# Kernel tuning notes

Measured on AMD Instinct MI355X. Metric: run time of the kernel, lower is better.

## Reference

```python
import jax, jax.numpy as jnp
import numpy as np

E, B, L, D = 3, 4, 1024, 768
DS = 64            # d_state
DI = 2 * D         # d_inner (expand=2)
DTR = 48           # dt_rank = ceil(D/16)
K = 4              # depthwise conv kernel size


def setup_inputs() -> dict:
    key = jax.random.key(0)
    ks = jax.random.split(key, 10)
    s = lambda i, shape, scale=0.02: (jax.random.normal(ks[i], shape, jnp.float32) * scale)
    A_log = jnp.broadcast_to(jnp.log(jnp.arange(1, DS + 1, dtype=jnp.float32)), (E, DI, DS))
    return {
        "base":   jax.random.normal(ks[0], (B, L, D), jnp.float32),
        "per_ch": jax.random.normal(ks[1], (E, B, L, D), jnp.float32),
        "alpha":  jnp.ones((E,), jnp.float32) / E,
        "ln_g":   jnp.ones((D,), jnp.float32),
        "ln_b":   jnp.zeros((D,), jnp.float32),
        "W_in":   s(2, (E, D, 2 * DI)),
        "conv_w": s(3, (E, DI, K), 0.1),
        "conv_b": jnp.zeros((E, DI), jnp.float32),
        "W_x":    s(4, (E, DI, DTR + 2 * DS)),
        "W_dt":   s(5, (E, DTR, DI), 0.05),
        "b_dt":   jnp.full((E, DI), -4.6, jnp.float32),  # softplus^-1(~0.01)
        "A_log":  A_log,
        "D_skip": jnp.ones((E, DI), jnp.float32),
        "W_out":  s(6, (E, DI, D)),
    }


def layer_norm(x, g, b, eps=1e-5):
    mu = jnp.mean(x, axis=-1, keepdims=True)
    var = jnp.mean(jnp.square(x - mu), axis=-1, keepdims=True)
    return (x - mu) * jax.lax.rsqrt(var + eps) * g + b


def mamba(x, W_in, conv_w, conv_b, W_x, W_dt, b_dt, A_log, D_skip, W_out):
    # x: [B, L, D]
    xz = x @ W_in                                   # [B, L, 2*DI]
    xp, z = jnp.split(xz, 2, axis=-1)               # each [B, L, DI]
    # causal depthwise conv along L
    xc = jnp.pad(xp, ((0, 0), (K - 1, 0), (0, 0)))
    xc = jax.lax.conv_general_dilated(
        jnp.swapaxes(xc, 1, 2),                     # [B, DI, L+K-1]
        conv_w[:, None, :],                         # [DI, 1, K]
        window_strides=(1,), padding='VALID',
        dimension_numbers=('NCH', 'OIH', 'NCH'),
        feature_group_count=DI)
    xc = jnp.swapaxes(xc, 1, 2) + conv_b            # [B, L, DI]
    xs = jax.nn.silu(xc)
    dbl = xs @ W_x                                  # [B, L, DTR+2*DS]
    dt, Bm, Cm = jnp.split(dbl, [DTR, DTR + DS], axis=-1)
    dt = jax.nn.softplus(dt @ W_dt + b_dt)          # [B, L, DI]
    A = -jnp.exp(A_log)                             # [DI, DS]

    def step(h, t):
        u_t, dt_t, B_t, C_t = t                     # [B,DI],[B,DI],[B,DS],[B,DS]
        dA = jnp.exp(dt_t[..., None] * A)           # [B, DI, DS]
        h = dA * h + (dt_t * u_t)[..., None] * B_t[:, None, :]
        y = jnp.einsum('bds,bs->bd', h, C_t)
        return h, y

    tm = lambda a: jnp.swapaxes(a, 0, 1)            # time-major
    h0 = jnp.zeros((x.shape[0], DI, DS), x.dtype)
    _, ys = jax.lax.scan(step, h0, (tm(xs), tm(dt), tm(Bm), tm(Cm)))
    y = jnp.swapaxes(ys, 0, 1) + xs * D_skip        # [B, L, DI]
    y = y * jax.nn.silu(z)
    return y @ W_out                                # [B, L, D]


def reference(base, per_ch, alpha, ln_g, ln_b, W_in, conv_w, conv_b, W_x,
              W_dt, b_dt, A_log, D_skip, W_out):
    w = jax.nn.softmax(alpha)                       # [E]
    xn = layer_norm(per_ch, ln_g, ln_b)             # shared LN on each channel
    outs = jax.vmap(mamba)(xn, W_in, conv_w, conv_b, W_x,
                           W_dt, b_dt, A_log, D_skip, W_out)  # [E, B, L, D]
    injection = jnp.einsum('e,ebld->bld', w, outs)
    return base + injection
```

## Files before the change

### kernel.cpp

```cpp
#include <hip/hip_runtime.h>
#include <hip/hip_bf16.h>

typedef __hip_bfloat16 bf16;
typedef unsigned short u16;
typedef __attribute__((ext_vector_type(8))) short s16x8;
typedef __attribute__((ext_vector_type(4))) short s16x4;
typedef __attribute__((ext_vector_type(4))) float f32x4;

#define EXP 3
#define BB  4
#define LL  1024
#define DD  768
#define DSN 64
#define DIN 1536
#define DTR 48
#define MM  4096

struct alignas(8)  bf16x4 { bf16 v[4]; };
struct alignas(16) bf16x8 { bf16 v[8]; };

__device__ __forceinline__ float siluf(float x) { return x / (1.f + __expf(-x)); }
__device__ __forceinline__ float softplusf(float x) { return (x > 15.f) ? x : log1pf(__expf(x)); }
__device__ __forceinline__ float bf2f(u16 h) { union { unsigned u; float f; } x; x.u = ((unsigned)h) << 16; return x.f; }

template <int CTRL>
__device__ __forceinline__ float ror_add(float x) {
  int y = __builtin_amdgcn_update_dpp(0, __float_as_int(x), CTRL, 0xf, 0xf, true);
  return x + __int_as_float(y);
}

__launch_bounds__(256)
__global__ void ln_apply_k(const float* __restrict__ pc, const float* __restrict__ lng,
                           const float* __restrict__ lnb, bf16* __restrict__ out) {
  int row  = blockIdx.x * 4 + (threadIdx.x >> 6);
  int lane = threadIdx.x & 63;
  const float* x = pc + (size_t)row * DD;
  float4 v[3];
  float s = 0.f, sq = 0.f;
#pragma unroll
  for (int i = 0; i < 3; i++) {
    v[i] = *(const float4*)(x + lane * 4 + i * 256);
    s  += v[i].x + v[i].y + v[i].z + v[i].w;
    sq += v[i].x * v[i].x + v[i].y * v[i].y + v[i].z * v[i].z + v[i].w * v[i].w;
  }
#pragma unroll
  for (int o = 1; o < 64; o <<= 1) { s += __shfl_xor(s, o); sq += __shfl_xor(sq, o); }
  float mu = s * (1.f / 768.f);
  float rs = rsqrtf(sq * (1.f / 768.f) - mu * mu + 1e-5f);
  bf16* op = out + (size_t)row * DD;
#pragma unroll
  for (int i = 0; i < 3; i++) {
    int col = lane * 4 + i * 256;
    float4 g4 = *(const float4*)(lng + col);
    float4 b4 = *(const float4*)(lnb + col);
    bf16x4 pk;
    pk.v[0] = (bf16)((v[i].x - mu) * rs * g4.x + b4.x);
    pk.v[1] = (bf16)((v[i].y - mu) * rs * g4.y + b4.y);
    pk.v[2] = (bf16)((v[i].z - mu) * rs * g4.z + b4.z);
    pk.v[3] = (bf16)((v[i].w - mu) * rs * g4.w + b4.w);
    *(bf16x4*)(op + col) = pk;
  }
}

__launch_bounds__(256)
__global__ void tcvt_k(const float* __restrict__ in, bf16* __restrict__ out,
                       int Ksrc, int ldin, int ldout,
                       size_t sIn, size_t sOut, int mode, const float* __restrict__ alphap) {
  __shared__ float tl[32][33];
  int z = blockIdx.z;
  const float* src = in + (size_t)z * sIn;
  bf16* dst = out + (size_t)z * sOut;
  int n0 = blockIdx.x * 32, k0 = blockIdx.y * 32;
  int tx = threadIdx.x, ty = threadIdx.y;
  int n = n0 + tx;
  int c = n; bool nv = true;
  if (mode == 1) {
    if (n < 48)       c = n;
    else if (n < 64)  nv = false;
    else if (n < 192) c = n - 16;
    else              nv = false;
  }
  float scale = 1.f;
  if (mode == 2) {
    float a0 = alphap[0], a1 = alphap[1], a2 = alphap[2];
    float mx = fmaxf(a0, fmaxf(a1, a2));
    float e0 = __expf(a0 - mx), e1 = __expf(a1 - mx), e2 = __expf(a2 - mx);
    scale = ((z == 0) ? e0 : (z == 1) ? e1 : e2) / (e0 + e1 + e2);
  }
#pragma unroll
  for (int i = 0; i < 32; i += 8) {
    int k = k0 + ty + i;
    float v = (nv && k < Ksrc) ? src[(size_t)k * ldin + c] : 0.f;
    tl[ty + i][tx] = v * scale;
  }
  __syncthreads();
#pragma unroll
  for (int i = 0; i < 32; i += 8) {
    dst[(size_t)(n0 + ty + i) * ldout + (k0 + tx)] = (bf16)tl[tx][ty + i];
  }
}

__launch_bounds__(256)
__global__ void conv_silu_k(const bf16* __restrict__ xp, const float* __restrict__ cw,
                            const float* __restrict__ cb, bf16* __restrict__ xs) {
  long i = ((long)blockIdx.x * 256 + threadIdx.x) * 8;
  int  c  = (int)(i % DIN);
  long rl = i / DIN;
  int  l  = (int)(rl & (LL - 1));
  int  e  = (int)(rl >> 12);
  const float* wp  = cw + (size_t)e * DIN * 4 + (size_t)c * 4;
  const float* cbp = cb + (size_t)e * DIN + c;
  float acc[8];
#pragma unroll
  for (int j = 0; j < 8; j++) acc[j] = cbp[j];
#pragma unroll
  for (int tap = 0; tap < 4; tap++) {
    if (l - 3 + tap >= 0) {
      s16x8 xv = *(const s16x8*)(const void*)(xp + (rl + tap - 3) * DIN + c);
#pragma unroll
      for (int j = 0; j < 8; j++)
        acc[j] = fmaf(bf2f((u16)xv[j]), wp[j * 4 + tap], acc[j]);
    }
  }
  bf16x8 pk;
#pragma unroll
  for (int j = 0; j < 8; j++) pk.v[j] = (bf16)siluf(acc[j]);
  *(bf16x8*)(xs + rl * DIN + c) = pk;
}

template<int MODE>
__launch_bounds__(256)
__global__ void mfma_gemm_k(const bf16* __restrict__ A, const bf16* __restrict__ Bt,
                            int Kdim, int lda,
                            size_t sA, size_t sB, size_t sO,
                            bf16* __restrict__ o0, bf16* __restrict__ o1,
                            const float* __restrict__ bias,
                            float* __restrict__ outp) {
  __shared__ short As[128 * 32];
  __shared__ short Bs[128 * 32];
  int z = blockIdx.z;
  A  += (size_t)z * sA;
  Bt += (size_t)z * sB;
  if (o0) o0 += (size_t)z * sO;
  if (o1) o1 += (size_t)z * sO;
  if constexpr (MODE == 1) outp += (size_t)z * (size_t)MM * 128;
  const float* bz = (MODE == 2) ? bias + (size_t)z * DIN : bias;

  int t = threadIdx.x;
  int l = t & 63, w = t >> 6;
  int wr = w >> 1, wc = w & 1;
  int n0 = blockIdx.x * 128, r0 = blockIdx.y * 128;

  int row = t >> 2, c3 = t & 3, col = c3 * 8;
  int plo = ((c3 & 1) ? 16 : 0) + ((c3 & 2) ? 4 : 0);
  int lrow = (l & 15) * 32 + (l >> 4) * 8;

  f32x4 acc[4][4] = {};

  for (int k0 = 0; k0 < Kdim; k0 += 32) {
    s16x8 va0 = *(const s16x8*)(const void*)(A  + (size_t)(r0 + row)      * lda  + k0 + col);
    s16x8 va1 = *(const s16x8*)(const void*)(A  + (size_t)(r0 + row + 64) * lda  + k0 + col);
    s16x8 vb0 = *(const s16x8*)(const void*)(Bt + (size_t)(n0 + row)      * Kdim + k0 + col);
    s16x8 vb1 = *(const s16x8*)(const void*)(Bt + (size_t)(n0 + row + 64) * Kdim + k0 + col);
    __syncthreads();
    *(s16x4*)(As + row * 32 + plo)          = __builtin_shufflevector(va0, va0, 0, 1, 2, 3);
    *(s16x4*)(As + row * 32 + plo + 8)      = __builtin_shufflevector(va0, va0, 4, 5, 6, 7);
    *(s16x4*)(As + (row + 64) * 32 + plo)     = __builtin_shufflevector(va1, va1, 0, 1, 2, 3);
    *(s16x4*)(As + (row + 64) * 32 + plo + 8) = __builtin_shufflevector(va1, va1, 4, 5, 6, 7);
    *(s16x4*)(Bs + row * 32 + plo)          = __builtin_shufflevector(vb0, vb0, 0, 1, 2, 3);
    *(s16x4*)(Bs + row * 32 + plo + 8)      = __builtin_shufflevector(vb0, vb0, 4, 5, 6, 7);
    *(s16x4*)(Bs + (row + 64) * 32 + plo)     = __builtin_shufflevector(vb1, vb1, 0, 1, 2, 3);
    *(s16x4*)(Bs + (row + 64) * 32 + plo + 8) = __builtin_shufflevector(vb1, vb1, 4, 5, 6, 7);
    __syncthreads();
    s16x8 af[4], bfv[4];
#pragma unroll
    for (int m = 0; m < 4; m++) af[m]  = *(const s16x8*)(As + (wr * 64 + m * 16) * 32 + lrow);
#pragma unroll
    for (int n = 0; n < 4; n++) bfv[n] = *(const s16x8*)(Bs + (wc * 64 + n * 16) * 32 + lrow);
#pragma unroll
    for (int m = 0; m < 4; m++)
#pragma unroll
      for (int n = 0; n < 4; n++)
        acc[m][n] = __builtin_amdgcn_mfma_f32_16x16x32_bf16(af[m], bfv[n], acc[m][n], 0, 0, 0);
  }

  int rb = r0 + wr * 64 + ((l >> 4) << 2);
  int cb = n0 + wc * 64 + (l & 15);
#pragma unroll
  for (int m = 0; m < 4; m++)
#pragma unroll
    for (int n = 0; n < 4; n++)
#pragma unroll
      for (int r = 0; r < 4; r++) {
        int gr = rb + m * 16 + r;
        int gc = cb + n * 16;
        float v = acc[m][n][r];
        if constexpr (MODE == 0) {
          if (n0 < DIN) o0[(size_t)gr * DIN + gc] = (bf16)v;
          else          o1[(size_t)gr * DIN + (gc - DIN)] = (bf16)siluf(v);
        } else if constexpr (MODE == 1) {
          if (gc < 64)       o0[(size_t)gr * 64 + gc] = (bf16)v;
          else if (gc < 192) outp[(size_t)gr * 128 + (gc - 64)] = v;
        } else if constexpr (MODE == 2) {
          o0[(size_t)gr * DIN + gc] = (bf16)softplusf(v + bz[gc]);
        } else {
          atomicAdd(&outp[(size_t)gr * DD + gc], v);
        }
      }
}

__launch_bounds__(256)
__global__ void copy4_k(const float* __restrict__ s, float* __restrict__ d, int n4) {
  int i = blockIdx.x * 256 + threadIdx.x;
  if (i < n4) ((float4*)d)[i] = ((const float4*)s)[i];
}

__launch_bounds__(256)
__global__ void scan_k(const bf16* __restrict__ dtb, bf16* __restrict__ xsb,
                       const bf16* __restrict__ gb, const float* __restrict__ dbl,
                       const float* __restrict__ A_log, const float* __restrict__ Dsk) {
  int gt = blockIdx.x * 256 + threadIdx.x;
  int sg = gt & 15;
  int cidx = gt >> 4;
  int d  = cidx % DIN;
  int eb = cidx / DIN;
  int e  = eb >> 2;

  float4 Ar = *(const float4*)(A_log + ((size_t)e * DIN + d) * DSN + sg * 4);
  const float LOG2E = 1.44269504088896f;
  float4 A2;
  A2.x = -__expf(Ar.x) * LOG2E;
  A2.y = -__expf(Ar.y) * LOG2E;
  A2.z = -__expf(Ar.z) * LOG2E;
  A2.w = -__expf(Ar.w) * LOG2E;
  float4 h = {0.f, 0.f, 0.f, 0.f};
  float dskip = Dsk[(size_t)e * DIN + d];

  unsigned idx  = (unsigned)eb * (LL * DIN) + (unsigned)d;
  unsigned bofs = (unsigned)eb * (LL * 128) + (unsigned)(sg * 4);

  float dtv = (float)dtb[idx];
  float u   = (float)xsb[idx];
  float gv  = (float)gb[idx];
  float4 Bv = *(const float4*)(dbl + bofs);
  float4 Cv = *(const float4*)(dbl + bofs + 64);

#pragma unroll 4
  for (int l = 0; l < LL; ++l) {
    unsigned idxn = idx + DIN;
    unsigned bofn = bofs + 128;
    float dtn = (float)dtb[idxn];
    float un  = (float)xsb[idxn];
    float gn  = (float)gb[idxn];
    float4 Bn = *(const float4*)(dbl + bofn);
    float4 Cn = *(const float4*)(dbl + bofn + 64);

    float du = dtv * u;
    float4 dA;
    dA.x = __builtin_amdgcn_exp2f(dtv * A2.x);
    dA.y = __builtin_amdgcn_exp2f(dtv * A2.y);
    dA.z = __builtin_amdgcn_exp2f(dtv * A2.z);
    dA.w = __builtin_amdgcn_exp2f(dtv * A2.w);
    h.x = fmaf(dA.x, h.x, du * Bv.x);
    h.y = fmaf(dA.y, h.y, du * Bv.y);
    h.z = fmaf(dA.z, h.z, du * Bv.z);
    h.w = fmaf(dA.w, h.w, du * Bv.w);
    float p = fmaf(h.x, Cv.x, fmaf(h.y, Cv.y, fmaf(h.z, Cv.z, h.w * Cv.w)));
    p = ror_add<0x128>(p);
    p = ror_add<0x124>(p);
    p = ror_add<0x122>(p);
    p = ror_add<0x121>(p);
    if (sg == 0) {
      xsb[idx] = (bf16)(fmaf(u, dskip, p) * gv);
    }
    idx = idxn; bofs = bofn;
    dtv = dtn; u = un; gv = gn; Bv = Bn; Cv = Cn;
  }
}

extern "C" void kernel_launch(void* const* d_in, const int* in_sizes, int n_in,
                              void* d_out, int out_size, void* d_ws, size_t ws_size,
                              hipStream_t stream) {
  const float* base   = (const float*)d_in[0];
  const float* per_ch = (const float*)d_in[1];
  const float* alpha  = (const float*)d_in[2];
  const float* ln_g   = (const float*)d_in[3];
  const float* ln_b   = (const float*)d_in[4];
  const float* W_in   = (const float*)d_in[5];
  const float* conv_w = (const float*)d_in[6];
  const float* conv_b = (const float*)d_in[7];
  const float* W_x    = (const float*)d_in[8];
  const float* W_dt   = (const float*)d_in[9];
  const float* b_dt   = (const float*)d_in[10];
  const float* A_log  = (const float*)d_in[11];
  const float* D_skip = (const float*)d_in[12];
  const float* W_out  = (const float*)d_in[13];
  float* out = (float*)d_out;
  (void)in_sizes; (void)n_in; (void)out_size; (void)ws_size;

  char* ws = (char*)d_ws;
  const size_t R = (size_t)EXP * MM * DIN * 2;
  bf16* Abf   = (bf16*)ws;
  bf16* xsws  = (bf16*)ws;
  bf16* gws   = (bf16*)(ws + R);
  bf16* dtws  = (bf16*)(ws + 2 * R);
  char* R4    = ws + 3 * R;
  bf16*  WinT  = (bf16*)R4;
  bf16*  WoutT = (bf16*)R4;
  float* dblf  = (float*)(R4 + 7077888);
  bf16* WxT   = (bf16*)(ws + 3 * R + 14155776);
  bf16* WdtT  = (bf16*)(ws + 3 * R + 14155776 + 2359296);
  bf16* dblp  = (bf16*)(ws + 3 * R + 14155776 + 2359296 + 589824);

  dim3 blk2(32, 8);

  ln_apply_k<<<EXP * BB * LL / 4, 256, 0, stream>>>(per_ch, ln_g, ln_b, Abf);
  tcvt_k<<<dim3(96, 24, EXP), blk2, 0, stream>>>(W_in, WinT, 768, 3072, 768,
        (size_t)768 * 3072, (size_t)3072 * 768, 0, nullptr);
  tcvt_k<<<dim3(8, 48, EXP), blk2, 0, stream>>>(W_x, WxT, 1536, 176, 1536,
        (size_t)1536 * 176, (size_t)256 * 1536, 1, nullptr);
  tcvt_k<<<dim3(48, 2, EXP), blk2, 0, stream>>>(W_dt, WdtT, 48, 1536, 64,
        (size_t)48 * 1536, (size_t)1536 * 64, 0, nullptr);

  mfma_gemm_k<0><<<dim3(24, 32, EXP), 256, 0, stream>>>(Abf, WinT, 768, DD,
        (size_t)MM * DD, (size_t)3072 * 768, (size_t)MM * DIN,
        dtws, gws, nullptr, nullptr);

  tcvt_k<<<dim3(24, 48, EXP), blk2, 0, stream>>>(W_out, WoutT, 1536, 768, 1536,
        (size_t)1536 * 768, (size_t)768 * 1536, 2, alpha);

  conv_silu_k<<<EXP * BB * LL * DIN / 8 / 256, 256, 0, stream>>>(dtws, conv_w, conv_b, xsws);

  mfma_gemm_k<1><<<dim3(2, 32, EXP), 256, 0, stream>>>(xsws, WxT, 1536, DIN,
        (size_t)MM * DIN, (size_t)256 * 1536, (size_t)MM * 64,
        dblp, nullptr, nullptr, dblf);

  mfma_gemm_k<2><<<dim3(12, 32, EXP), 256, 0, stream>>>(dblp, WdtT, 64, 64,
        (size_t)MM * 64, (size_t)1536 * 64, (size_t)MM * DIN,
        dtws, nullptr, b_dt, nullptr);

  copy4_k<<<MM * DD / 4 / 256, 256, 0, stream>>>(base, out, MM * DD / 4);
  scan_k<<<EXP * BB * DIN * 16 / 256, 256, 0, stream>>>(dtws, xsws, gws, dblf, A_log, D_skip);
  mfma_gemm_k<3><<<dim3(6, 32, EXP), 256, 0, stream>>>(xsws, WoutT, 1536, DIN,
        (size_t)MM * DIN, (size_t)768 * 1536, 0,
        nullptr, nullptr, nullptr, out);
}
```

Before: 898.3 us.

## Fuse silu(z) gating into output GEMM and deepen GEMM K-step to 64

The out-projection GEMM now multiplies its A tiles by the silu(z) gate while loading, so the scan kernel no longer reads the gate tensor each timestep. All MFMA GEMMs also stage 64-wide K slices per iteration instead of 32, halving the barrier and loop overhead per K. This doubles shared memory per block, raises register pressure and may lower occupancy. It also adds an extra bf16 rounding of the gated product.

```diff
diff --git a/kernel.cpp b/kernel.cpp
--- a/kernel.cpp
+++ b/kernel.cpp
@@ -22,6 +22,17 @@
 __device__ __forceinline__ float siluf(float x) { return x / (1.f + __expf(-x)); }
 __device__ __forceinline__ float softplusf(float x) { return (x > 15.f) ? x : log1pf(__expf(x)); }
 __device__ __forceinline__ float bf2f(u16 h) { union { unsigned u; float f; } x; x.u = ((unsigned)h) << 16; return x.f; }
+
+__device__ __forceinline__ s16x8 gmul8(s16x8 a, s16x8 g) {
+  s16x8 r;
+#pragma unroll
+  for (int j = 0; j < 8; j++) {
+    union { bf16 b; u16 u; } cv;
+    cv.b = (bf16)(bf2f((u16)a[j]) * bf2f((u16)g[j]));
+    r[j] = (short)cv.u;
+  }
+  return r;
+}
 
 template <int CTRL>
 __device__ __forceinline__ float ror_add(float x) {
@@ -135,15 +146,17 @@
                             size_t sA, size_t sB, size_t sO,
                             bf16* __restrict__ o0, bf16* __restrict__ o1,
                             const float* __restrict__ bias,
-                            float* __restrict__ outp) {
-  __shared__ short As[128 * 32];
-  __shared__ short Bs[128 * 32];
+                            float* __restrict__ outp,
+                            const bf16* __restrict__ gat) {
+  __shared__ short As[128 * 64];
+  __shared__ short Bs[128 * 64];
   int z = blockIdx.z;
   A  += (size_t)z * sA;
   Bt += (size_t)z * sB;
   if (o0) o0 += (size_t)z * sO;
   if (o1) o1 += (size_t)z * sO;
   if constexpr (MODE == 1) outp += (size_t)z * (size_t)MM * 128;
+  if constexpr (MODE == 3) gat += (size_t)z * sA;
   const float* bz = (MODE == 2) ? bias + (size_t)z * DIN : bias;
 
   int t = threadIdx.x;
@@ -157,32 +170,51 @@
 
   f32x4 acc[4][4] = {};
 
-  for (int k0 = 0; k0 < Kdim; k0 += 32) {
-    s16x8 va0 = *(const s16x8*)(const void*)(A  + (size_t)(r0 + row)      * lda  + k0 + col);
-    s16x8 va1 = *(const s16x8*)(const void*)(A  + (size_t)(r0 + row + 64) * lda  + k0 + col);
-    s16x8 vb0 = *(const s16x8*)(const void*)(Bt + (size_t)(n0 + row)      * Kdim + k0 + col);
-    s16x8 vb1 = *(const s16x8*)(const void*)(Bt + (size_t)(n0 + row + 64) * Kdim + k0 + col);
+#define PUT(DST, ROW, V)                                                        \
+  { *(s16x4*)((DST) + (ROW) * 32 + plo)     = __builtin_shufflevector(V, V, 0, 1, 2, 3); \
+    *(s16x4*)((DST) + (ROW) * 32 + plo + 8) = __builtin_shufflevector(V, V, 4, 5, 6, 7); }
+
+  for (int k0 = 0; k0 < Kdim; k0 += 64) {
+    const bf16* pa = A  + (size_t)(r0 + row) * lda  + k0 + col;
+    const bf16* pb = Bt + (size_t)(n0 + row) * Kdim + k0 + col;
+    s16x8 va0 = *(const s16x8*)(const void*)(pa);
+    s16x8 va1 = *(const s16x8*)(const void*)(pa + (size_t)64 * lda);
+    s16x8 va2 = *(const s16x8*)(const void*)(pa + 32);
+    s16x8 va3 = *(const s16x8*)(const void*)(pa + (size_t)64 * lda + 32);
+    s16x8 vb0 = *(const s16x8*)(const void*)(pb);
+    s16x8 vb1 = *(const s16x8*)(const void*)(pb + (size_t)64 * Kdim);
+    s16x8 vb2 = *(const s16x8*)(const void*)(pb + 32);
+    s16x8 vb3 = *(const s16x8*)(const void*)(pb + (size_t)64 * Kdim + 32);
+    if constexpr (MODE == 3) {
+      const bf16* pg = gat + (size_t)(r0 + row) * lda + k0 + col;
+      va0 = gmul8(va0, *(const s16x8*)(const void*)(pg));
+      va1 = gmul8(va1, *(const s16x8*)(const void*)(pg + (size_t)64 * lda));
+      va2 = gmul8(va2, *(const s16x8*)(const void*)(pg + 32));
+      va3 = gmul8(va3, *(const s16x8*)(const void*)(pg + (size_t)64 * lda + 32));
+    }
     __syncthreads();
-    *(s16x4*)(As + row * 32 + plo)          = __builtin_shufflevector(va0, va0, 0, 1, 2, 3);
-    *(s16x4*)(As + row * 32 + plo + 8)      = __builtin_shufflevector(va0, va0, 4, 5, 6, 7);
-    *(s16x4*)(As + (row + 64) * 32 + plo)     = __builtin_shufflevector(va1, va1, 0, 1, 2, 3);
-    *(s16x4*)(As + (row + 64) * 32 + plo + 8) = __builtin_shufflevector(va1, va1, 4, 5, 6, 7);
-    *(s16x4*)(Bs + row * 32 + plo)          = __builtin_shufflevector(vb0, vb0, 0, 1, 2, 3);
-    *(s16x4*)(Bs + row * 32 + plo + 8)      = __builtin_shufflevector(vb0, vb0, 4, 5, 6, 7);
-    *(s16x4*)(Bs + (row + 64) * 32 + plo)     = __builtin_shufflevector(vb1, vb1, 0, 1, 2, 3);
-    *(s16x4*)(Bs + (row + 64) * 32 + plo + 8) = __builtin_shufflevector(vb1, vb1, 4, 5, 6, 7);
+    PUT(As, row, va0)  PUT(As, row + 64, va1)
+    PUT(As + 4096, row, va2)  PUT(As + 4096, row + 64, va3)
+    PUT(Bs, row, vb0)  PUT(Bs, row + 64, vb1)
+    PUT(Bs + 4096, row, vb2)  PUT(Bs + 4096, row + 64, vb3)
     __syncthreads();
-    s16x8 af[4], bfv[4];
-#pragma unroll
-    for (int m = 0; m < 4; m++) af[m]  = *(const s16x8*)(As + (wr * 64 + m * 16) * 32 + lrow);
-#pragma unroll
-    for (int n = 0; n < 4; n++) bfv[n] = *(const s16x8*)(Bs + (wc * 64 + n * 16) * 32 + lrow);
-#pragma unroll
-    for (int m = 0; m < 4; m++)
-#pragma unroll
-      for (int n = 0; n < 4; n++)
-        acc[m][n] = __builtin_amdgcn_mfma_f32_16x16x32_bf16(af[m], bfv[n], acc[m][n], 0, 0, 0);
-  }
+#pragma unroll
+    for (int p = 0; p < 2; p++) {
+      const short* as = As + p * 4096;
+      const short* bs = Bs + p * 4096;
+      s16x8 af[4], bfv[4];
+#pragma unroll
+      for (int m = 0; m < 4; m++) af[m]  = *(const s16x8*)(as + (wr * 64 + m * 16) * 32 + lrow);
+#pragma unroll
+      for (int n = 0; n < 4; n++) bfv[n] = *(const s16x8*)(bs + (wc * 64 + n * 16) * 32 + lrow);
+#pragma unroll
+      for (int m = 0; m < 4; m++)
+#pragma unroll
+        for (int n = 0; n < 4; n++)
+          acc[m][n] = __builtin_amdgcn_mfma_f32_16x16x32_bf16(af[m], bfv[n], acc[m][n], 0, 0, 0);
+    }
+  }
+#undef PUT
 
   int rb = r0 + wr * 64 + ((l >> 4) << 2);
   int cb = n0 + wc * 64 + (l & 15);
@@ -217,7 +249,7 @@
 
 __launch_bounds__(256)
 __global__ void scan_k(const bf16* __restrict__ dtb, bf16* __restrict__ xsb,
-                       const bf16* __restrict__ gb, const float* __restrict__ dbl,
+                       const float* __restrict__ dbl,
                        const float* __restrict__ A_log, const float* __restrict__ Dsk) {
   int gt = blockIdx.x * 256 + threadIdx.x;
   int sg = gt & 15;
@@ -241,7 +273,6 @@
 
   float dtv = (float)dtb[idx];
   float u   = (float)xsb[idx];
-  float gv  = (float)gb[idx];
   float4 Bv = *(const float4*)(dbl + bofs);
   float4 Cv = *(const float4*)(dbl + bofs + 64);
 
@@ -251,7 +282,6 @@
     unsigned bofn = bofs + 128;
     float dtn = (float)dtb[idxn];
     float un  = (float)xsb[idxn];
-    float gn  = (float)gb[idxn];
     float4 Bn = *(const float4*)(dbl + bofn);
     float4 Cn = *(const float4*)(dbl + bofn + 64);
 
@@ -271,10 +301,10 @@
     p = ror_add<0x122>(p);
     p = ror_add<0x121>(p);
     if (sg == 0) {
-      xsb[idx] = (bf16)(fmaf(u, dskip, p) * gv);
+      xsb[idx] = (bf16)fmaf(u, dskip, p);
     }
     idx = idxn; bofs = bofn;
-    dtv = dtn; u = un; gv = gn; Bv = Bn; Cv = Cn;
+    dtv = dtn; u = un; Bv = Bn; Cv = Cn;
   }
 }
 
@@ -324,7 +354,7 @@
 
   mfma_gemm_k<0><<<dim3(24, 32, EXP), 256, 0, stream>>>(Abf, WinT, 768, DD,
         (size_t)MM * DD, (size_t)3072 * 768, (size_t)MM * DIN,
-        dtws, gws, nullptr, nullptr);
+        dtws, gws, nullptr, nullptr, nullptr);
 
   tcvt_k<<<dim3(24, 48, EXP), blk2, 0, stream>>>(W_out, WoutT, 1536, 768, 1536,
         (size_t)1536 * 768, (size_t)768 * 1536, 2, alpha);
@@ -333,15 +363,15 @@
 
   mfma_gemm_k<1><<<dim3(2, 32, EXP), 256, 0, stream>>>(xsws, WxT, 1536, DIN,
         (size_t)MM * DIN, (size_t)256 * 1536, (size_t)MM * 64,
-        dblp, nullptr, nullptr, dblf);
+        dblp, nullptr, nullptr, dblf, nullptr);
 
   mfma_gemm_k<2><<<dim3(12, 32, EXP), 256, 0, stream>>>(dblp, WdtT, 64, 64,
         (size_t)MM * 64, (size_t)1536 * 64, (size_t)MM * DIN,
-        dtws, nullptr, b_dt, nullptr);
+        dtws, nullptr, b_dt, nullptr, nullptr);
 
   copy4_k<<<MM * DD / 4 / 256, 256, 0, stream>>>(base, out, MM * DD / 4);
-  scan_k<<<EXP * BB * DIN * 16 / 256, 256, 0, stream>>>(dtws, xsws, gws, dblf, A_log, D_skip);
+  scan_k<<<EXP * BB * DIN * 16 / 256, 256, 0, stream>>>(dtws, xsws, dblf, A_log, D_skip);
   mfma_gemm_k<3><<<dim3(6, 32, EXP), 256, 0, stream>>>(xsws, WoutT, 1536, DIN,
         (size_t)MM * DIN, (size_t)768 * 1536, 0,
-        nullptr, nullptr, nullptr, out);
-}
+        nullptr, nullptr, nullptr, out, gws);
+}
```

Measured after the change: 879.1 us. 1.02x faster.

## Fuse silu gate multiply into output GEMM load and use fast softplus

Applied to the files above, without the earlier changes.

Moves the gating multiply from the sequential scan kernel into the A-tile load path of the output projection GEMM. This reduces per-timestep global loads in the latency-bound scan. Softplus is rewritten with hardware exp2/log intrinsics in a numerically stable form. In exchange, the GEMM reads the gate tensor once per column block and does extra bf16 conversions in its load loop.

```diff
diff --git a/kernel.cpp b/kernel.cpp
--- a/kernel.cpp
+++ b/kernel.cpp
@@ -20,8 +20,24 @@
 struct alignas(16) bf16x8 { bf16 v[8]; };
 
 __device__ __forceinline__ float siluf(float x) { return x / (1.f + __expf(-x)); }
-__device__ __forceinline__ float softplusf(float x) { return (x > 15.f) ? x : log1pf(__expf(x)); }
 __device__ __forceinline__ float bf2f(u16 h) { union { unsigned u; float f; } x; x.u = ((unsigned)h) << 16; return x.f; }
+
+__device__ __forceinline__ float softplusf(float x) {
+  const float LOG2E = 1.44269504088896f, LN2 = 0.69314718055995f;
+  float t = __builtin_amdgcn_exp2f(-fabsf(x) * LOG2E);
+  return fmaxf(x, 0.f) + LN2 * __builtin_amdgcn_logf(1.f + t);
+}
+
+__device__ __forceinline__ s16x8 gmul8(s16x8 a, s16x8 g) {
+  s16x8 r;
+#pragma unroll
+  for (int j = 0; j < 8; j++) {
+    union { bf16 b; u16 u; } cv;
+    cv.b = (bf16)(bf2f((u16)a[j]) * bf2f((u16)g[j]));
+    r[j] = (short)cv.u;
+  }
+  return r;
+}
 
 template <int CTRL>
 __device__ __forceinline__ float ror_add(float x) {
@@ -135,7 +151,8 @@
                             size_t sA, size_t sB, size_t sO,
                             bf16* __restrict__ o0, bf16* __restrict__ o1,
                             const float* __restrict__ bias,
-                            float* __restrict__ outp) {
+                            float* __restrict__ outp,
+                            const bf16* __restrict__ gat) {
   __shared__ short As[128 * 32];
   __shared__ short Bs[128 * 32];
   int z = blockIdx.z;
@@ -144,6 +161,7 @@
   if (o0) o0 += (size_t)z * sO;
   if (o1) o1 += (size_t)z * sO;
   if constexpr (MODE == 1) outp += (size_t)z * (size_t)MM * 128;
+  if constexpr (MODE == 3) gat += (size_t)z * sA;
   const float* bz = (MODE == 2) ? bias + (size_t)z * DIN : bias;
 
   int t = threadIdx.x;
@@ -162,6 +180,11 @@
     s16x8 va1 = *(const s16x8*)(const void*)(A  + (size_t)(r0 + row + 64) * lda  + k0 + col);
     s16x8 vb0 = *(const s16x8*)(const void*)(Bt + (size_t)(n0 + row)      * Kdim + k0 + col);
     s16x8 vb1 = *(const s16x8*)(const void*)(Bt + (size_t)(n0 + row + 64) * Kdim + k0 + col);
+    if constexpr (MODE == 3) {
+      const bf16* pg = gat + (size_t)(r0 + row) * lda + k0 + col;
+      va0 = gmul8(va0, *(const s16x8*)(const void*)(pg));
+      va1 = gmul8(va1, *(const s16x8*)(const void*)(pg + (size_t)64 * lda));
+    }
     __syncthreads();
     *(s16x4*)(As + row * 32 + plo)          = __builtin_shufflevector(va0, va0, 0, 1, 2, 3);
     *(s16x4*)(As + row * 32 + plo + 8)      = __builtin_shufflevector(va0, va0, 4, 5, 6, 7);
@@ -217,7 +240,7 @@
 
 __launch_bounds__(256)
 __global__ void scan_k(const bf16* __restrict__ dtb, bf16* __restrict__ xsb,
-                       const bf16* __restrict__ gb, const float* __restrict__ dbl,
+                       const float* __restrict__ dbl,
                        const float* __restrict__ A_log, const float* __restrict__ Dsk) {
   int gt = blockIdx.x * 256 + threadIdx.x;
   int sg = gt & 15;
@@ -241,7 +264,6 @@
 
   float dtv = (float)dtb[idx];
   float u   = (float)xsb[idx];
-  float gv  = (float)gb[idx];
   float4 Bv = *(const float4*)(dbl + bofs);
   float4 Cv = *(const float4*)(dbl + bofs + 64);
 
@@ -251,7 +273,6 @@
     unsigned bofn = bofs + 128;
     float dtn = (float)dtb[idxn];
     float un  = (float)xsb[idxn];
-    float gn  = (float)gb[idxn];
     float4 Bn = *(const float4*)(dbl + bofn);
     float4 Cn = *(const float4*)(dbl + bofn + 64);
 
@@ -271,10 +292,10 @@
     p = ror_add<0x122>(p);
     p = ror_add<0x121>(p);
     if (sg == 0) {
-      xsb[idx] = (bf16)(fmaf(u, dskip, p) * gv);
+      xsb[idx] = (bf16)fmaf(u, dskip, p);
     }
     idx = idxn; bofs = bofn;
-    dtv = dtn; u = un; gv = gn; Bv = Bn; Cv = Cn;
+    dtv = dtn; u = un; Bv = Bn; Cv = Cn;
   }
 }
 
@@ -324,7 +345,7 @@
 
   mfma_gemm_k<0><<<dim3(24, 32, EXP), 256, 0, stream>>>(Abf, WinT, 768, DD,
         (size_t)MM * DD, (size_t)3072 * 768, (size_t)MM * DIN,
-        dtws, gws, nullptr, nullptr);
+        dtws, gws, nullptr, nullptr, nullptr);
 
   tcvt_k<<<dim3(24, 48, EXP), blk2, 0, stream>>>(W_out, WoutT, 1536, 768, 1536,
         (size_t)1536 * 768, (size_t)768 * 1536, 2, alpha);
@@ -333,15 +354,15 @@
 
   mfma_gemm_k<1><<<dim3(2, 32, EXP), 256, 0, stream>>>(xsws, WxT, 1536, DIN,
         (size_t)MM * DIN, (size_t)256 * 1536, (size_t)MM * 64,
-        dblp, nullptr, nullptr, dblf);
+        dblp, nullptr, nullptr, dblf, nullptr);
 
   mfma_gemm_k<2><<<dim3(12, 32, EXP), 256, 0, stream>>>(dblp, WdtT, 64, 64,
         (size_t)MM * 64, (size_t)1536 * 64, (size_t)MM * DIN,
-        dtws, nullptr, b_dt, nullptr);
+        dtws, nullptr, b_dt, nullptr, nullptr);
 
   copy4_k<<<MM * DD / 4 / 256, 256, 0, stream>>>(base, out, MM * DD / 4);
-  scan_k<<<EXP * BB * DIN * 16 / 256, 256, 0, stream>>>(dtws, xsws, gws, dblf, A_log, D_skip);
+  scan_k<<<EXP * BB * DIN * 16 / 256, 256, 0, stream>>>(dtws, xsws, dblf, A_log, D_skip);
   mfma_gemm_k<3><<<dim3(6, 32, EXP), 256, 0, stream>>>(xsws, WoutT, 1536, DIN,
         (size_t)MM * DIN, (size_t)768 * 1536, 0,
-        nullptr, nullptr, nullptr, out);
-}
+        nullptr, nullptr, nullptr, out, gws);
+}
```

Result: faster. 840.6 us (-6.4%).
